# Performance work log

Measured on AMD Instinct MI355X. Metric: run time of the kernel, lower is better.

The kernel has to match this reference:

```python
import jax, jax.numpy as jnp
import numpy as np

GRID_SIZE = 16          # number of spline intervals; G+1 = 17 control points
KH, KW = 3, 3           # kernel size
EPS = 1e-8


def _extract_patches(x, kh, kw):
    """x: (B,H,W,C) -> patches (B,Ho,Wo,C,kh,kw), valid padding, stride 1."""
    B, H, W, C = x.shape
    Ho, Wo = H - kh + 1, W - kw + 1
    rows = []
    for i in range(kh):
        cols = []
        for j in range(kw):
            cols.append(x[:, i:i + Ho, j:j + Wo, :])  # (B,Ho,Wo,C)
        rows.append(jnp.stack(cols, axis=-1))          # (B,Ho,Wo,C,kw)
    return jnp.stack(rows, axis=-2)                    # (B,Ho,Wo,C,kh,kw)


def setup_inputs() -> dict:
    key = jax.random.key(0)
    k1, k2, k3, k4 = jax.random.split(key, 4)
    B, H, W, C, F = 4, 66, 66, 32, 64
    x = jax.random.normal(k1, (B, H, W, C), dtype=jnp.float32)
    control_points = jax.random.normal(k2, (F, C, KH, KW, GRID_SIZE + 1), dtype=jnp.float32) * 0.1
    w_spline = jax.random.normal(k3, (F, C, KH, KW), dtype=jnp.float32) * 0.1
    w_silu = jax.random.normal(k4, (F, C, KH, KW), dtype=jnp.float32) * 0.1
    bias = jnp.zeros((F,), dtype=jnp.float32)
    return {"x": x, "control_points": control_points, "w_spline": w_spline,
            "w_silu": w_silu, "bias": bias}


def reference(x, control_points, w_spline, w_silu, bias):
    # Fixed B-spline grid in [-1, 1]
    grid = jnp.linspace(-1.0, 1.0, GRID_SIZE + 1, dtype=x.dtype)  # (G+1,)
    grid_spacing = 2.0 / GRID_SIZE

    # Patch extraction (valid padding, stride 1)
    patches = _extract_patches(x, KH, KW)  # (B,Ho,Wo,C,kh,kw)

    # Linear B-spline (hat) basis with normalization
    xc = jnp.clip(patches, -1.0, 1.0)
    dist = jnp.abs(xc[..., None] - grid)                     # (B,Ho,Wo,C,kh,kw,G+1)
    w = jnp.maximum(0.0, 1.0 - dist / grid_spacing)
    basis = w / (jnp.sum(w, axis=-1, keepdims=True) + EPS)

    # K(x) = w_spline * spline(x) + w_silu * SiLU(x); reduce over (C,kh,kw) per filter
    cp_eff = w_spline[..., None] * control_points            # (F,C,kh,kw,G+1)
    spline_term = jnp.einsum('bhwcijg,fcijg->bhwf', basis, cp_eff)
    silu_term = jnp.einsum('bhwcij,fcij->bhwf', jax.nn.silu(patches), w_silu)

    return spline_term + silu_term + bias  # (B,Ho,Wo,F)
```

## Files before the change

### kernel.cpp

```cpp
#include <hip/hip_runtime.h>
#include <stdint.h>

typedef _Float16 half8 __attribute__((ext_vector_type(8)));
typedef float f32x16 __attribute__((ext_vector_type(16)));
typedef float f32x4  __attribute__((ext_vector_type(4)));

#define NTH2 340992
#define PREP_BLOCKS (NTH2 / 256)

__global__ __launch_bounds__(256) void kan_prep(
    const float* __restrict__ cp, const float* __restrict__ wspl,
    const float* __restrict__ wsil, _Float16* __restrict__ th2)
{
    int e  = blockIdx.x * 256 + threadIdx.x;
    int p  = e / 18944;
    int r  = e - p * 18944;
    int f  = r / 296;
    int cb = r - f * 296;
    int i  = p / 6;
    int jh = p - i * 6;
    int j  = jh >> 1;
    int h2 = jh & 1;
    float v = 0.0f;
    if (cb < 288) {
        int kk = h2 * 288 + cb;
        int c  = kk / 18;
        int m  = kk - c * 18;
        int base = ((f * 32 + c) * 3 + i) * 3 + j;
        v = (m < 17) ? wspl[base] * cp[base * 17 + m] : wsil[base];
    }
    th2[e] = (_Float16)v;
}

__global__ __launch_bounds__(256, 1) void kan_main(
    const float* __restrict__ x, const _Float16* __restrict__ th2,
    const float* __restrict__ bias, float* __restrict__ out)
{
    __shared__ __align__(16) _Float16 lA[66 * 584];
    __shared__ __align__(16) _Float16 lB[2][64 * 296];

    const int bx = blockIdx.x;
    const int b  = bx >> 6;
    const int ho = bx & 63;

    const int tid  = threadIdx.x;
    const int wv   = tid >> 6;
    const int wpx  = wv >> 1;
    const int wf   = wv & 1;
    const int lane = tid & 63;
    const int r31  = lane & 31;
    const int kh   = lane >> 5;

    const int srow = tid >> 2;
    const int oct  = tid & 3;
    const int erow = 64 + (tid >> 5);
    const int ec   = tid & 31;

    const char* thB = (const char*)th2;

#define STAGE(lp, bi)                                                          \
    {                                                                          \
        const char* gs = thB + (size_t)(bi) * 37888 + lane * 16;               \
        char* ls = (char*)(lp);                                                \
        _Pragma("unroll")                                                      \
        for (int t = 0; t < 10; ++t) {                                         \
            int u = wv + 4 * t;                                                \
            if (u < 37)                                                        \
                __builtin_amdgcn_global_load_lds(                              \
                    (const __attribute__((address_space(1))) void*)(gs + u * 1024), \
                    (__attribute__((address_space(3))) void*)(ls + u * 1024),  \
                    16, 0, 0);                                                 \
        }                                                                      \
    }

    STAGE(lB[0], 0)

    f32x16 acc;
    {
        float bv = bias[wf * 32 + r31];
#pragma unroll
        for (int r = 0; r < 16; ++r) acc[r] = bv;
    }

    for (int i = 0; i < 3; ++i) {
        const float* xr =
            x + ((size_t)((b * 66 + ho + i) * 66 + srow)) * 32 + oct * 8;
        f32x4 x0 = *(const f32x4*)(xr);
        f32x4 x1 = *(const f32x4*)(xr + 4);
        float xev = (tid < 64)
            ? x[((size_t)((b * 66 + ho + i) * 66 + erow)) * 32 + ec] : 0.0f;

#pragma unroll
        for (int q = 0; q < 6; ++q) {
            const int J  = q >> 1;
            const int H2 = q & 1;
            const bool last = (q == 5) && (i == 2);

            if (q < 5) { STAGE(lB[(q + 1) & 1], i * 6 + q + 1) }
            else if (i < 2) { STAGE(lB[0], (i + 1) * 6) }

            if (q == 0) {
                char* abase = (char*)lA + srow * 1168 + oct * 288;
#pragma unroll
                for (int np = 0; np < 4; ++np) {
                    union { _Float16 h[36]; uint64_t qq[9]; } pk;
#pragma unroll
                    for (int d = 0; d < 2; ++d) {
                        const int n = np * 2 + d;
                        float pv = (n < 4) ? x0[n] : x1[n - 4];
                        float u  = fmaf(fminf(1.0f, fmaxf(-1.0f, pv)), 8.0f, 8.0f);
#pragma unroll
                        for (int m = 0; m < 17; ++m)
                            pk.h[d * 18 + m] =
                                (_Float16)fmaxf(0.0f, 1.0f - fabsf(u - (float)m));
                        pk.h[d * 18 + 17] = (_Float16)(
                            pv * __builtin_amdgcn_rcpf(1.0f + __expf(-pv)));
                    }
                    uint64_t* dst = (uint64_t*)(abase + np * 72);
#pragma unroll
                    for (int r = 0; r < 9; ++r) dst[r] = pk.qq[r];
                }
                if (tid < 64) {
                    union { _Float16 h[18]; uint32_t w[9]; } ew;
                    float pv = xev;
                    float u  = fmaf(fminf(1.0f, fmaxf(-1.0f, pv)), 8.0f, 8.0f);
#pragma unroll
                    for (int m = 0; m < 17; ++m)
                        ew.h[m] = (_Float16)fmaxf(0.0f, 1.0f - fabsf(u - (float)m));
                    ew.h[17] = (_Float16)(
                        pv * __builtin_amdgcn_rcpf(1.0f + __expf(-pv)));
                    uint32_t* dst = (uint32_t*)((char*)lA + erow * 1168 + ec * 36);
#pragma unroll
                    for (int r = 0; r < 9; ++r) dst[r] = ew.w[r];
                }
            }

            if (last)            asm volatile("s_waitcnt vmcnt(0) lgkmcnt(0)" ::: "memory");
            else if (wv == 0)    asm volatile("s_waitcnt vmcnt(10) lgkmcnt(0)" ::: "memory");
            else                 asm volatile("s_waitcnt vmcnt(9) lgkmcnt(0)" ::: "memory");
            __builtin_amdgcn_s_barrier();
            __builtin_amdgcn_sched_barrier(0);

            const _Float16* pa =
                lA + (wpx * 32 + r31 + J) * 584 + H2 * 288 + kh * 8;
            const _Float16* pb = lB[q & 1] + (wf * 32 + r31) * 296 + kh * 8;
#pragma unroll
            for (int s = 0; s < 18; ++s) {
                half8 a  = *(const half8*)(pa + s * 16);
                half8 bf = *(const half8*)(pb + s * 16);
                acc = __builtin_amdgcn_mfma_f32_32x32x16_f16(a, bf, acc, 0, 0, 0);
            }

            asm volatile("s_waitcnt lgkmcnt(0)" ::: "memory");
            __builtin_amdgcn_s_barrier();
        }
    }
#undef STAGE

    float* obase = out
        + ((size_t)((b * 64 + ho) * 64 + wpx * 32)) * 64 + wf * 32;
#pragma unroll
    for (int r = 0; r < 16; ++r) {
        int rowD = (r & 3) + 8 * (r >> 2) + 4 * kh;
        obase[(size_t)rowD * 64 + r31] = acc[r];
    }
}

extern "C" void kernel_launch(void* const* d_in, const int* in_sizes, int n_in,
                              void* d_out, int out_size, void* d_ws, size_t ws_size,
                              hipStream_t stream) {
    const float* x    = (const float*)d_in[0];
    const float* cp   = (const float*)d_in[1];
    const float* wspl = (const float*)d_in[2];
    const float* wsil = (const float*)d_in[3];
    const float* bias = (const float*)d_in[4];
    float* out = (float*)d_out;

    _Float16* th2 = (_Float16*)d_ws;

    kan_prep<<<PREP_BLOCKS, 256, 0, stream>>>(cp, wspl, wsil, th2);
    kan_main<<<256, 256, 0, stream>>>(x, th2, bias, out);
}
```

Baseline: 88.44 us.

## Split output row across two blocks with smaller LDS, drop double buffering

The main kernel now launches 512 blocks of 128 threads, each covering half an output row (32 pixels × 64 filters) instead of 256 blocks of 256 threads covering a full row. LDS shrinks to a single B buffer and a 32-row A tile, and the A basis is recomputed per (i,j,h2) step rather than once per kernel row. The aim is more blocks and better occupancy across the CUs. In exchange it drops the async double-buffered weight prefetch in favour of load-then-syncthreads, and it recomputes the basis and weight loads more often.

```diff
diff --git a/kernel.cpp b/kernel.cpp
--- a/kernel.cpp
+++ b/kernel.cpp
@@ -32,48 +32,31 @@
     th2[e] = (_Float16)v;
 }
 
-__global__ __launch_bounds__(256, 1) void kan_main(
+__global__ __launch_bounds__(128) void kan_main(
     const float* __restrict__ x, const _Float16* __restrict__ th2,
     const float* __restrict__ bias, float* __restrict__ out)
 {
-    __shared__ __align__(16) _Float16 lA[66 * 584];
-    __shared__ __align__(16) _Float16 lB[2][64 * 296];
+    __shared__ __align__(16) _Float16 lA[32 * 296];
+    __shared__ __align__(16) _Float16 lB[64 * 296];
 
-    const int bx = blockIdx.x;
-    const int b  = bx >> 6;
-    const int ho = bx & 63;
+    const int bx  = blockIdx.x;
+    const int ph  = bx >> 8;
+    const int row = bx & 255;
+    const int b   = row >> 6;
+    const int ho  = row & 63;
 
     const int tid  = threadIdx.x;
-    const int wv   = tid >> 6;
-    const int wpx  = wv >> 1;
-    const int wf   = wv & 1;
+    const int wf   = tid >> 6;
     const int lane = tid & 63;
     const int r31  = lane & 31;
     const int kh   = lane >> 5;
 
-    const int srow = tid >> 2;
-    const int oct  = tid & 3;
-    const int erow = 64 + (tid >> 5);
-    const int ec   = tid & 31;
+    const int ar = tid >> 2;
+    const int cq = tid & 3;
 
     const char* thB = (const char*)th2;
-
-#define STAGE(lp, bi)                                                          \
-    {                                                                          \
-        const char* gs = thB + (size_t)(bi) * 37888 + lane * 16;               \
-        char* ls = (char*)(lp);                                                \
-        _Pragma("unroll")                                                      \
-        for (int t = 0; t < 10; ++t) {                                         \
-            int u = wv + 4 * t;                                                \
-            if (u < 37)                                                        \
-                __builtin_amdgcn_global_load_lds(                              \
-                    (const __attribute__((address_space(1))) void*)(gs + u * 1024), \
-                    (__attribute__((address_space(3))) void*)(ls + u * 1024),  \
-                    16, 0, 0);                                                 \
-        }                                                                      \
-    }
-
-    STAGE(lB[0], 0)
+    char* lBc = (char*)lB;
+    char* lAc = (char*)lA;
 
     f32x16 acc;
     {
@@ -82,83 +65,69 @@
         for (int r = 0; r < 16; ++r) acc[r] = bv;
     }
 
-    for (int i = 0; i < 3; ++i) {
-        const float* xr =
-            x + ((size_t)((b * 66 + ho + i) * 66 + srow)) * 32 + oct * 8;
-        f32x4 x0 = *(const f32x4*)(xr);
-        f32x4 x1 = *(const f32x4*)(xr + 4);
-        float xev = (tid < 64)
-            ? x[((size_t)((b * 66 + ho + i) * 66 + erow)) * 32 + ec] : 0.0f;
+    const _Float16* pa = lA + r31 * 296 + kh * 8;
+    const _Float16* pb = lB + (wf * 32 + r31) * 296 + kh * 8;
 
+    for (int p = 0; p < 18; ++p) {
+        const int i  = p / 6;
+        const int jh = p - i * 6;
+        const int j  = jh >> 1;
+        const int h2 = jh & 1;
+
+        {
+            const char* gs = thB + (size_t)p * 37888 + wf * 1024 + lane * 16;
+            char* ld = lBc + wf * 1024;
 #pragma unroll
-        for (int q = 0; q < 6; ++q) {
-            const int J  = q >> 1;
-            const int H2 = q & 1;
-            const bool last = (q == 5) && (i == 2);
+            for (int t = 0; t < 18; ++t)
+                __builtin_amdgcn_global_load_lds(
+                    (const __attribute__((address_space(1))) void*)(gs + t * 2048),
+                    (__attribute__((address_space(3))) void*)(ld + t * 2048),
+                    16, 0, 0);
+            if (wf == 0)
+                __builtin_amdgcn_global_load_lds(
+                    (const __attribute__((address_space(1))) void*)(gs + 36864),
+                    (__attribute__((address_space(3))) void*)(lBc + 36864),
+                    16, 0, 0);
+        }
 
-            if (q < 5) { STAGE(lB[(q + 1) & 1], i * 6 + q + 1) }
-            else if (i < 2) { STAGE(lB[0], (i + 1) * 6) }
-
-            if (q == 0) {
-                char* abase = (char*)lA + srow * 1168 + oct * 288;
+        {
+            const f32x4 xv = *(const f32x4*)(
+                x + ((size_t)((b * 66 + ho + i) * 66 + ph * 32 + ar + j)) * 32
+                  + h2 * 16 + cq * 4);
 #pragma unroll
-                for (int np = 0; np < 4; ++np) {
-                    union { _Float16 h[36]; uint64_t qq[9]; } pk;
+            for (int pr = 0; pr < 2; ++pr) {
+                union { _Float16 h[36]; uint64_t q[9]; } pk;
 #pragma unroll
-                    for (int d = 0; d < 2; ++d) {
-                        const int n = np * 2 + d;
-                        float pv = (n < 4) ? x0[n] : x1[n - 4];
-                        float u  = fmaf(fminf(1.0f, fmaxf(-1.0f, pv)), 8.0f, 8.0f);
-#pragma unroll
-                        for (int m = 0; m < 17; ++m)
-                            pk.h[d * 18 + m] =
-                                (_Float16)fmaxf(0.0f, 1.0f - fabsf(u - (float)m));
-                        pk.h[d * 18 + 17] = (_Float16)(
-                            pv * __builtin_amdgcn_rcpf(1.0f + __expf(-pv)));
-                    }
-                    uint64_t* dst = (uint64_t*)(abase + np * 72);
-#pragma unroll
-                    for (int r = 0; r < 9; ++r) dst[r] = pk.qq[r];
-                }
-                if (tid < 64) {
-                    union { _Float16 h[18]; uint32_t w[9]; } ew;
-                    float pv = xev;
+                for (int d = 0; d < 2; ++d) {
+                    float pv = xv[pr * 2 + d];
                     float u  = fmaf(fminf(1.0f, fmaxf(-1.0f, pv)), 8.0f, 8.0f);
 #pragma unroll
                     for (int m = 0; m < 17; ++m)
-                        ew.h[m] = (_Float16)fmaxf(0.0f, 1.0f - fabsf(u - (float)m));
-                    ew.h[17] = (_Float16)(
+                        pk.h[d * 18 + m] =
+                            (_Float16)fmaxf(0.0f, 1.0f - fabsf(u - (float)m));
+                    pk.h[d * 18 + 17] = (_Float16)(
                         pv * __builtin_amdgcn_rcpf(1.0f + __expf(-pv)));
-                    uint32_t* dst = (uint32_t*)((char*)lA + erow * 1168 + ec * 36);
+                }
+                uint64_t* dst = (uint64_t*)(lAc + ar * 592 + cq * 144 + pr * 72);
 #pragma unroll
-                    for (int r = 0; r < 9; ++r) dst[r] = ew.w[r];
-                }
+                for (int r = 0; r < 9; ++r) dst[r] = pk.q[r];
             }
+        }
 
-            if (last)            asm volatile("s_waitcnt vmcnt(0) lgkmcnt(0)" ::: "memory");
-            else if (wv == 0)    asm volatile("s_waitcnt vmcnt(10) lgkmcnt(0)" ::: "memory");
-            else                 asm volatile("s_waitcnt vmcnt(9) lgkmcnt(0)" ::: "memory");
-            __builtin_amdgcn_s_barrier();
-            __builtin_amdgcn_sched_barrier(0);
+        __syncthreads();
 
-            const _Float16* pa =
-                lA + (wpx * 32 + r31 + J) * 584 + H2 * 288 + kh * 8;
-            const _Float16* pb = lB[q & 1] + (wf * 32 + r31) * 296 + kh * 8;
 #pragma unroll
-            for (int s = 0; s < 18; ++s) {
-                half8 a  = *(const half8*)(pa + s * 16);
-                half8 bf = *(const half8*)(pb + s * 16);
-                acc = __builtin_amdgcn_mfma_f32_32x32x16_f16(a, bf, acc, 0, 0, 0);
-            }
+        for (int s = 0; s < 18; ++s) {
+            half8 a  = *(const half8*)(pa + s * 16);
+            half8 bf = *(const half8*)(pb + s * 16);
+            acc = __builtin_amdgcn_mfma_f32_32x32x16_f16(a, bf, acc, 0, 0, 0);
+        }
 
-            asm volatile("s_waitcnt lgkmcnt(0)" ::: "memory");
-            __builtin_amdgcn_s_barrier();
-        }
+        __syncthreads();
     }
-#undef STAGE
 
     float* obase = out
-        + ((size_t)((b * 64 + ho) * 64 + wpx * 32)) * 64 + wf * 32;
+        + ((size_t)((b * 64 + ho) * 64 + ph * 32)) * 64 + wf * 32;
 #pragma unroll
     for (int r = 0; r < 16; ++r) {
         int rowD = (r & 3) + 8 * (r >> 2) + 4 * kh;
@@ -179,5 +148,5 @@
     _Float16* th2 = (_Float16*)d_ws;
 
     kan_prep<<<PREP_BLOCKS, 256, 0, stream>>>(cp, wspl, wsil, th2);
-    kan_main<<<256, 256, 0, stream>>>(x, th2, bias, out);
+    kan_main<<<512, 128, 0, stream>>>(x, th2, bias, out);
 }
```

Result: slower. 100.5 us (+13.6%).
